# Kernel tuning notes

Hardware: AMD Instinct MI355X
Metric: run time of the kernel (lower is better)

Reference implementation:

```python
import jax, jax.numpy as jnp
import numpy as np

FEAT_STRIDE = 16
PRE_NMS_TOP_N = 6000
POST_NMS_TOP_N = 300
NMS_THRESH = 0.7
MIN_SIZE = 16.0
SCALES = np.array([8.0, 16.0, 32.0])
RATIOS = np.array([0.5, 1.0, 2.0])


def _whctrs(a):
    w = a[2] - a[0] + 1.0
    h = a[3] - a[1] + 1.0
    return w, h, a[0] + 0.5 * (w - 1.0), a[1] + 0.5 * (h - 1.0)


def _mkanchors(ws, hs, xc, yc):
    ws = np.asarray(ws).reshape(-1, 1)
    hs = np.asarray(hs).reshape(-1, 1)
    return np.hstack([xc - 0.5 * (ws - 1.0), yc - 0.5 * (hs - 1.0),
                      xc + 0.5 * (ws - 1.0), yc + 0.5 * (hs - 1.0)])


def generate_anchors(base_size, ratios, scales):
    base = np.array([1.0, 1.0, base_size, base_size]) - 1.0
    w, h, xc, yc = _whctrs(base)
    size = w * h
    ws = np.round(np.sqrt(size / ratios))
    hs = np.round(ws * ratios)
    ratio_anchors = _mkanchors(ws, hs, xc, yc)
    out = []
    for i in range(ratio_anchors.shape[0]):
        w, h, xc, yc = _whctrs(ratio_anchors[i])
        out.append(_mkanchors(w * scales, h * scales, xc, yc))
    return np.vstack(out)


def _nms(boxes, scores, thresh, max_out):
    # greedy NMS, boxes [N,4], scores [N] (-inf = invalid). Returns idx [max_out], valid [max_out]
    N = boxes.shape[0]
    x1, y1, x2, y2 = boxes[:, 0], boxes[:, 1], boxes[:, 2], boxes[:, 3]
    areas = (x2 - x1 + 1.0) * (y2 - y1 + 1.0)
    ar = jnp.arange(N)

    def step(s, _):
        i = jnp.argmax(s)
        valid = s[i] > -jnp.inf
        b = boxes[i]
        xx1 = jnp.maximum(b[0], x1)
        yy1 = jnp.maximum(b[1], y1)
        xx2 = jnp.minimum(b[2], x2)
        yy2 = jnp.minimum(b[3], y2)
        inter = jnp.maximum(0.0, xx2 - xx1 + 1.0) * jnp.maximum(0.0, yy2 - yy1 + 1.0)
        iou = inter / (areas[i] + areas - inter)
        sup = (iou > thresh) | (ar == i)
        return jnp.where(sup, -jnp.inf, s), (i, valid)

    _, (idx, valid) = jax.lax.scan(step, scores, None, length=max_out)
    return idx, valid


def setup_inputs() -> dict:
    key = jax.random.key(0)
    k1, k2 = jax.random.split(key)
    B, A, Hf, Wf = 16, 9, 160, 160
    scores_map = jax.random.uniform(k1, (B, 2 * A, Hf, Wf), dtype=jnp.float32)
    bbox_deltas = jax.random.normal(k2, (B, 4 * A, Hf, Wf), dtype=jnp.float32) * 0.2
    im_info = jnp.tile(jnp.array([[Hf * FEAT_STRIDE, Wf * FEAT_STRIDE, 1.0]], jnp.float32), (B, 1))
    return {"scores_map": scores_map, "bbox_deltas": bbox_deltas, "im_info": im_info}


def reference(scores_map, bbox_deltas, im_info):
    anchors0 = jnp.asarray(generate_anchors(16, RATIOS, SCALES), jnp.float32)  # [A,4]
    A = anchors0.shape[0]
    B, _, Hf, Wf = scores_map.shape
    # fg scores: [B, A, H, W] -> [B, H*W*A]
    scores = scores_map[:, A:].transpose(0, 2, 3, 1).reshape(B, -1)
    deltas = bbox_deltas.transpose(0, 2, 3, 1).reshape(B, -1, 4)  # [B, H*W*A, 4]
    sx = (jnp.arange(Wf) * FEAT_STRIDE).astype(jnp.float32)
    sy = (jnp.arange(Hf) * FEAT_STRIDE).astype(jnp.float32)
    SX, SY = jnp.meshgrid(sx, sy)  # [H, W]
    shifts = jnp.stack([SX.ravel(), SY.ravel(), SX.ravel(), SY.ravel()], axis=1)  # [K,4]
    all_anchors = (shifts[:, None, :] + anchors0[None, :, :]).reshape(-1, 4)  # [K*A, 4]

    aw = all_anchors[:, 2] - all_anchors[:, 0] + 1.0
    ah = all_anchors[:, 3] - all_anchors[:, 1] + 1.0
    acx = all_anchors[:, 0] + 0.5 * aw
    acy = all_anchors[:, 1] + 0.5 * ah

    def single(s, d, info):
        # bbox_transform_inv
        pcx = d[:, 0] * aw + acx
        pcy = d[:, 1] * ah + acy
        pw = jnp.exp(d[:, 2]) * aw
        ph = jnp.exp(d[:, 3]) * ah
        x1 = jnp.clip(pcx - 0.5 * pw, 0.0, info[1] - 1.0)
        y1 = jnp.clip(pcy - 0.5 * ph, 0.0, info[0] - 1.0)
        x2 = jnp.clip(pcx + 0.5 * pw, 0.0, info[1] - 1.0)
        y2 = jnp.clip(pcy + 0.5 * ph, 0.0, info[0] - 1.0)
        boxes = jnp.stack([x1, y1, x2, y2], axis=1)
        ms = MIN_SIZE * info[2]
        keep = ((x2 - x1 + 1.0) >= ms) & ((y2 - y1 + 1.0) >= ms)
        s = jnp.where(keep, s, -jnp.inf)
        top_s, top_i = jax.lax.top_k(s, PRE_NMS_TOP_N)
        top_b = boxes[top_i]
        idx, valid = _nms(top_b, top_s, NMS_THRESH, POST_NMS_TOP_N)
        return jnp.where(valid[:, None], top_b[idx], 0.0)  # [POST, 4]

    out_boxes = jax.vmap(single)(scores, deltas, im_info)  # [B, POST, 4]
    batch_col = jnp.broadcast_to(
        jnp.arange(B, dtype=out_boxes.dtype)[:, None, None], (B, POST_NMS_TOP_N, 1))
    return jnp.concatenate([batch_col, out_boxes], axis=2)  # [B, POST, 5]
```

## Files before the change

kernel.cpp:

```cpp
#include <hip/hip_runtime.h>
#include <cstdint>
#include <cstddef>

typedef unsigned int u32;
typedef unsigned short u16;
typedef unsigned long long u64;

#define NBATCH 16
#define NA 9
#define HF 160
#define WF 160
#define HWC (HF*WF)
#define NPB (NA*HWC)
#define PRE_N 6000
#define POST_N 300
#define SEL_CAP 8192
#define NBIN 2048
#define UNI_BINS 2048
#define NMS_W 16
#define CHUNK 512

__constant__ float c_AW[9] = {184.f,368.f,736.f,128.f,256.f,512.f,88.f,176.f,352.f};
__constant__ float c_AH[9] = {96.f,192.f,384.f,128.f,256.f,512.f,176.f,352.f,704.f};

__device__ __forceinline__ void box_core(
    float d0, float d1, float d2, float d3, int a, int x, int y,
    float imH, float imW, float ms,
    float& x1, float& y1, float& x2, float& y2, bool& keep)
{
  float aw = c_AW[a], ah = c_AH[a];
  float acx = (float)x * 16.0f + 8.0f;
  float acy = (float)y * 16.0f + 8.0f;
  float pcx = d0 * aw + acx;
  float pcy = d1 * ah + acy;
  float pw  = expf(d2) * aw;
  float ph  = expf(d3) * ah;
  x1 = fminf(fmaxf(pcx - 0.5f * pw, 0.0f), imW - 1.0f);
  y1 = fminf(fmaxf(pcy - 0.5f * ph, 0.0f), imH - 1.0f);
  x2 = fminf(fmaxf(pcx + 0.5f * pw, 0.0f), imW - 1.0f);
  y2 = fminf(fmaxf(pcy + 0.5f * ph, 0.0f), imH - 1.0f);
  keep = ((x2 - x1 + 1.0f) >= ms) && ((y2 - y1 + 1.0f) >= ms);
}

__device__ __forceinline__ void box_from_deltas(
    const float* __restrict__ bd, int b, int a, int pos,
    float imH, float imW, float ms,
    float& x1, float& y1, float& x2, float& y2, bool& keep)
{
  int y = pos / WF;
  int x = pos - y * WF;
  size_t base = ((size_t)(b * 4 * NA) + 4 * a) * HWC + (size_t)pos;
  float d0 = bd[base];
  float d1 = bd[base + HWC];
  float d2 = bd[base + 2 * HWC];
  float d3 = bd[base + 3 * HWC];
  box_core(d0, d1, d2, d3, a, x, y, imH, imW, ms, x1, y1, x2, y2, keep);
}

__device__ __forceinline__ u32 desc_enc(float s) {
  u32 su = __float_as_uint(s);
  u32 asc = (su & 0x80000000u) ? ~su : (su | 0x80000000u);
  return ~asc;
}

__device__ __forceinline__ bool iou_gt(float inter, float uni) {
  float ss = fmaf(0.7f, uni, -inter);
  if (fabsf(ss) <= uni * 1e-6f) return (inter / uni > 0.7f);
  return ss < 0.0f;
}

__global__ void __launch_bounds__(256) k_scores_hist(
    const float* __restrict__ sm, const float* __restrict__ bd,
    const float* __restrict__ info, u32* __restrict__ keys, u32* __restrict__ hist) {
  __shared__ u32 lh[UNI_BINS];
  int img   = blockIdx.x / 45;
  int rem   = blockIdx.x - img * 45;
  int a     = rem / 5;
  int chunk = rem - a * 5;
  int tid = threadIdx.x;
  for (int i = tid; i < UNI_BINS; i += 256) lh[i] = 0;
  __syncthreads();
  float imH = info[img*3+0], imW = info[img*3+1], ms = 16.0f * info[img*3+2];
  const float* sp = sm + ((size_t)(img * 2 * NA) + NA + a) * HWC;
  const float* dp = bd + ((size_t)(img * 4 * NA) + 4 * a) * HWC;
  u32* kp = keys + (size_t)img * NPB + (size_t)a * HWC;
  for (int j = 0; j < 5; j++) {
    int pos0 = (chunk * 1280 + j * 256 + tid) * 4;
    float4 s4  = *(const float4*)&sp[pos0];
    float4 q0  = *(const float4*)&dp[pos0];
    float4 q1  = *(const float4*)&dp[HWC + pos0];
    float4 q2  = *(const float4*)&dp[2*HWC + pos0];
    float4 q3  = *(const float4*)&dp[3*HWC + pos0];
    float sv[4] = {s4.x, s4.y, s4.z, s4.w};
    float v0[4] = {q0.x, q0.y, q0.z, q0.w};
    float v1[4] = {q1.x, q1.y, q1.z, q1.w};
    float v2[4] = {q2.x, q2.y, q2.z, q2.w};
    float v3[4] = {q3.x, q3.y, q3.z, q3.w};
    u32 kq[4];
    #pragma unroll
    for (int e = 0; e < 4; e++) {
      int pos = pos0 + e;
      int y = pos / WF;
      int x = pos - y * WF;
      float x1, y1, x2, y2; bool keep;
      box_core(v0[e], v1[e], v2[e], v3[e], a, x, y, imH, imW, ms, x1, y1, x2, y2, keep);
      float s = sv[e];
      if (!keep) s = __uint_as_float(0xFF800000u);
      kq[e] = desc_enc(s);
      int q = (int)floorf(s * (float)UNI_BINS);
      q = q < 0 ? 0 : (q > UNI_BINS - 1 ? UNI_BINS - 1 : q);
      atomicAdd(&lh[(UNI_BINS - 1) - q], 1u);
    }
    *(uint4*)&kp[pos0] = make_uint4(kq[0], kq[1], kq[2], kq[3]);
  }
  __syncthreads();
  u32* gh = hist + img * UNI_BINS;
  for (int i = tid; i < UNI_BINS; i += 256) { u32 v = lh[i]; if (v) atomicAdd(&gh[i], v); }
}

__global__ void __launch_bounds__(256) k_select(
    const u32* __restrict__ keys, const u32* __restrict__ hist, u64* __restrict__ thresh_arr) {
  int img = blockIdx.x, tid = threadIdx.x;
  __shared__ u32 sc[256];
  __shared__ u32 lh[NBIN];
  __shared__ u64 sh_thresh;
  __shared__ int sh_state;
  __shared__ u64 sh_prefix;
  __shared__ u32 sh_kth;
  const u32* gh = hist + img * UNI_BINS;
  u32 loc[8]; u32 tot = 0;
  for (int j = 0; j < 8; j++) { loc[j] = gh[tid * 8 + j]; tot += loc[j]; }
  if (tid == 0) { sh_state = 0; sh_prefix = 0; sh_kth = PRE_N; }
  sc[tid] = tot;
  __syncthreads();
  for (int off = 1; off < 256; off <<= 1) {
    u32 v = sc[tid]; u32 a = (tid >= off) ? sc[tid - off] : 0u;
    __syncthreads(); sc[tid] = v + a; __syncthreads();
  }
  u32 incl = sc[tid], excl = incl - tot;
  if (PRE_N > excl && PRE_N <= incl) {
    u32 run = excl;
    for (int j = 0; j < 8; j++) {
      run += loc[j];
      if (run >= PRE_N) {
        int b = tid * 8 + j;
        if (b < UNI_BINS - 1 && run <= SEL_CAP) {
          float sb = (float)(UNI_BINS - 1 - b) * (1.0f / (float)UNI_BINS);
          sh_thresh = ((u64)desc_enc(sb) << 32) | 0xFFFFFFFFull;
          sh_state = 1;
        }
        break;
      }
    }
  }
  __syncthreads();
  if (!sh_state) {
    const u32* kp = keys + (size_t)img * NPB;
    const int shifts[6] = {53, 42, 31, 20, 9, 0};
    const int widths[6] = {11, 11, 11, 11, 11, 9};
    for (int p = 0; p < 6; p++) {
      if (sh_state) break;
      for (int i = tid; i < NBIN; i += 256) lh[i] = 0;
      __syncthreads();
      u64 prefix = sh_prefix; u32 kth = sh_kth;
      int shift = shifts[p], width = widths[p];
      u32 nb = 1u << width;
      int hs = shift + width;
      for (int i = tid; i < NPB; i += 256) {
        int a = i / HWC;
        int pos = i - a * HWC;
        u64 key = ((u64)kp[i] << 32) | (u64)(u32)(pos * NA + a);
        bool m = (p == 0) || ((key >> hs) == prefix);
        if (m) atomicAdd(&lh[(u32)(key >> shift) & (nb - 1u)], 1u);
      }
      __syncthreads();
      u32 l2[8]; u32 t2 = 0;
      for (int j = 0; j < 8; j++) {
        u32 b = (u32)(tid * 8 + j);
        u32 v = (b < nb) ? lh[b] : 0u;
        l2[j] = v; t2 += v;
      }
      sc[tid] = t2; __syncthreads();
      for (int off = 1; off < 256; off <<= 1) {
        u32 v = sc[tid]; u32 a = (tid >= off) ? sc[tid - off] : 0u;
        __syncthreads(); sc[tid] = v + a; __syncthreads();
      }
      u32 incl2 = sc[tid], excl2 = incl2 - t2;
      if (kth > excl2 && kth <= incl2) {
        u32 run = excl2;
        for (int j = 0; j < 8; j++) {
          run += l2[j];
          if (run >= kth) {
            u32 bin = (u32)(tid * 8 + j);
            u32 below = run - l2[j];
            u32 cnt = l2[j];
            u32 knew = kth - below;
            u64 pfull = (prefix << width) | (u64)bin;
            u32 M = (u32)PRE_N - knew + cnt;
            if (M <= SEL_CAP) {
              u64 lowmask = (shift > 0) ? ((1ULL << shift) - 1ULL) : 0ULL;
              sh_thresh = (pfull << shift) | lowmask;
              sh_state = 1;
            } else {
              sh_prefix = pfull; sh_kth = knew;
            }
            break;
          }
        }
      }
      __syncthreads();
    }
  }
  if (tid == 0) thresh_arr[img] = sh_thresh;
}

__global__ void __launch_bounds__(256) k_compact(
    const u32* __restrict__ keys, const u64* __restrict__ thresh,
    u32* __restrict__ selcnt, u64* __restrict__ sel,
    const float* __restrict__ bd, const float* __restrict__ info,
    float4* __restrict__ boxsel) {
  int img = blockIdx.y;
  int tid = threadIdx.x;
  u64 T = thresh[img];
  int t0 = blockIdx.x * 3840;
  const u32* kp = keys + (size_t)img * NPB + t0;
  u64 fk[15];
  u32 mycnt = 0;
  #pragma unroll
  for (int j = 0; j < 15; j++) {
    int t = t0 + j * 256 + tid;
    u32 d = kp[j * 256 + tid];
    int a = t / HWC;
    int pos = t - a * HWC;
    u64 key = ((u64)d << 32) | (u64)(u32)(pos * NA + a);
    fk[j] = key;
    if (key <= T) mycnt++;
  }
  __shared__ u32 sc[256];
  __shared__ u32 sbase;
  sc[tid] = mycnt;
  __syncthreads();
  for (int off = 1; off < 256; off <<= 1) {
    u32 v = sc[tid];
    u32 add = (tid >= off) ? sc[tid - off] : 0u;
    __syncthreads();
    sc[tid] = v + add;
    __syncthreads();
  }
  if (tid == 255 && sc[255] > 0) sbase = atomicAdd(&selcnt[img], sc[255]);
  __syncthreads();
  if (mycnt == 0) return;
  u32 myoff = sbase + sc[tid] - mycnt;
  u64* sp = sel + (size_t)img * SEL_CAP;
  float4* bp = boxsel + (size_t)img * SEL_CAP;
  float imH = info[img*3+0], imW = info[img*3+1], ms = 16.0f * info[img*3+2];
  u32 c = 0;
  #pragma unroll
  for (int j = 0; j < 15; j++) {
    u64 key = fk[j];
    if (key <= T) {
      u32 p = myoff + c;
      if (p < SEL_CAP) {
        u32 desc = (u32)(key >> 32);
        u32 idx = (u32)key;
        sp[p] = ((u64)desc << 31) | ((u64)idx << 13) | (u64)p;
        int a = (int)(idx % NA);
        int pos = (int)(idx / NA);
        float x1, y1, x2, y2; bool keep;
        box_from_deltas(bd, img, a, pos, imH, imW, ms, x1, y1, x2, y2, keep);
        bp[p] = make_float4(x1, y1, x2, y2);
      }
      c++;
    }
  }
}

__global__ void __launch_bounds__(256) k_sort1(u64* __restrict__ sel, const u32* __restrict__ selcnt) {
  __shared__ u64 s[CHUNK];
  int img = blockIdx.y, c = blockIdx.x, tid = threadIdx.x;
  u32 cnt = selcnt[img]; if (cnt > SEL_CAP) cnt = SEL_CAP;
  u64* sp = sel + (size_t)img * SEL_CAP + (size_t)c * CHUNK;
  int gbase = c * CHUNK;
  for (int i = tid; i < CHUNK; i += 256) s[i] = ((u32)(gbase + i) < cnt) ? sp[i] : ~0ULL;
  __syncthreads();
  for (int k = 2; k <= CHUNK; k <<= 1) {
    for (int j = k >> 1; j > 0; j >>= 1) {
      for (int i = tid; i < CHUNK; i += 256) {
        int p = i ^ j;
        if (p > i) {
          u64 a = s[i], b = s[p];
          bool up = ((i & k) == 0);
          if (up ? (a > b) : (a < b)) { s[i] = b; s[p] = a; }
        }
      }
      __syncthreads();
    }
  }
  for (int i = tid; i < CHUNK; i += 256) sp[i] = s[i];
}

__global__ void __launch_bounds__(1024) k_sort2nms(
    const u64* __restrict__ sel, const u32* __restrict__ selcnt,
    const float4* __restrict__ boxsel, float* __restrict__ out) {
  union SB {
    u64 s[SEL_CAP];
    struct {
      u16 slot16[PRE_N + 64];
      float4 kbox[POST_N];
      float karea[POST_N];
      u64 kcodeW[(POST_N + 7) / 8];
      float4 cb[2][64];
      float car[2][64];
      int cint[2][64];
      u64 wcol[2][64];
      u64 supw[2][NMS_W];
    } n;
  };
  __shared__ SB u;
  __shared__ int sh_nv;
  __shared__ int sh_nkept;
  int img = blockIdx.x;
  int tid = threadIdx.x;
  const u64* sp = sel + (size_t)img * SEL_CAP;
  if (tid == 0) { sh_nv = PRE_N; sh_nkept = 0; }
  for (int i = tid; i < SEL_CAP; i += 1024) u.s[i] = sp[i];
  __syncthreads();
  int d0 = tid * 8;
  for (int L = CHUNK; L < SEL_CAP; L <<= 1) {
    int pairBase = d0 & ~(2 * L - 1);
    int d = d0 - pairBase;
    const u64* A = u.s + pairBase;
    const u64* B = u.s + pairBase + L;
    int lo = d - L; if (lo < 0) lo = 0;
    int hi = (d < L) ? d : L;
    while (lo < hi) {
      int mid = (lo + hi) >> 1;
      if (A[mid] <= B[d - 1 - mid]) lo = mid + 1; else hi = mid;
    }
    int ia = lo, ib = d - lo;
    u64 o[8];
    #pragma unroll
    for (int k = 0; k < 8; k++) {
      bool ta = (ib >= L) || (ia < L && A[ia] <= B[ib]);
      o[k] = ta ? A[ia++] : B[ib++];
    }
    __syncthreads();
    #pragma unroll
    for (int k = 0; k < 8; k++) u.s[d0 + k] = o[k];
    __syncthreads();
  }
  u64 rv[6];
  {
    int k = 0;
    for (int r = tid; r < PRE_N; r += 1024, k++) rv[k] = u.s[r];
    __syncthreads();
    k = 0;
    for (int r = tid; r < PRE_N; r += 1024, k++) {
      u64 key = rv[k];
      u32 desc = (u32)(key >> 31);
      bool valid = desc < 0xFF800000u;
      if (!valid) atomicMin(&sh_nv, r);
      u.n.slot16[r] = valid ? (u16)(key & 0x1FFFu) : (u16)0xFFFF;
    }
  }
  __syncthreads();
  int lane = tid & 63;
  int wv = tid >> 6;
  int nvalid = sh_nv;
  if (nvalid > PRE_N) nvalid = PRE_N;
  const float4* bp = boxsel + (size_t)img * SEL_CAP;
  if (tid < 64) {
    float4 c = make_float4(0.f, 0.f, 0.f, 0.f);
    if (tid < nvalid) { u16 sl = u.n.slot16[tid]; c = bp[sl]; }
    u.n.cb[0][tid] = c;
    float A = (c.z - c.x + 1.0f) * (c.w - c.y + 1.0f);
    u.n.car[0][tid] = A;
    u.n.cint[0][tid] = (int)rintf(8.0f * log2f(A));
  } else if (tid < 128) {
    u.n.wcol[0][tid - 64] = 0;
  } else if (tid < 128 + NMS_W) {
    u.n.supw[0][tid - 128] = 0;
  }
  __syncthreads();
  int pb = 0;
  for (int base = 0; base < nvalid; base += 64, pb ^= 1) {
    int nk = sh_nkept;
    if (nk >= POST_N) break;
    int bn = nvalid - base; if (bn > 64) bn = 64;
    bool sup;
    u64 colpart = 0;
    {
      bool inb = lane < bn;
      sup = !inb;
      if (inb) {
        float4 C = u.n.cb[pb][lane];
        float A0 = u.n.car[pb][lane];
        int myc = u.n.cint[pb][lane];
        int nw = (nk + 7) >> 3;
        for (int jw = wv; jw < nw; jw += NMS_W) {
          u64 w = u.n.kcodeW[jw];
          int jbase = jw << 3;
          int jm = nk - jbase; if (jm > 8) jm = 8;
          for (int k = 0; k < jm; k++) {
            int d = (int)((w >> (k * 8)) & 0xFFu) - myc;
            if (d > 5 || d < -5) continue;
            int j = jbase + k;
            float4 K = u.n.kbox[j];
            float xx1 = fmaxf(K.x, C.x);
            float yy1 = fmaxf(K.y, C.y);
            float xx2 = fminf(K.z, C.z);
            float yy2 = fminf(K.w, C.w);
            float iw = fmaxf(0.0f, xx2 - xx1 + 1.0f);
            float ih = fmaxf(0.0f, yy2 - yy1 + 1.0f);
            float inter = iw * ih;
            float uni = (u.n.karea[j] + A0) - inter;
            sup = sup | iou_gt(inter, uni);
          }
        }
        for (int i = wv; i < lane; i += NMS_W) {
          if (i >= bn) break;
          float Ai = u.n.car[pb][i];
          if (Ai <= 0.6999f * A0 || A0 <= 0.6999f * Ai) continue;
          float4 I4 = u.n.cb[pb][i];
          float xx1 = fmaxf(I4.x, C.x);
          float yy1 = fmaxf(I4.y, C.y);
          float xx2 = fminf(I4.z, C.z);
          float yy2 = fminf(I4.w, C.w);
          float iw = fmaxf(0.0f, xx2 - xx1 + 1.0f);
          float ih = fmaxf(0.0f, yy2 - yy1 + 1.0f);
          float inter = iw * ih;
          float uni = (Ai + A0) - inter;
          if (iou_gt(inter, uni)) colpart |= 1ULL << i;
        }
      }
    }
    u64 bm = __ballot(sup);
    if (lane == 0) u.n.supw[pb][wv] = bm;
    if (colpart) atomicOr(&u.n.wcol[pb][lane], colpart);
    __syncthreads();
    if (wv == 0) {
      u64 so = (lane < NMS_W) ? u.n.supw[pb][lane] : 0ULL;
      so |= __shfl_xor(so, 1);
      so |= __shfl_xor(so, 2);
      so |= __shfl_xor(so, 4);
      so |= __shfl_xor(so, 8);
      so = __shfl(so, 0);
      u64 validm = (bn >= 64) ? ~0ULL : ((1ULL << bn) - 1ULL);
      u64 colm = u.n.wcol[pb][lane];
      u64 live = validm & ~so;
      u64 km = 0;
      int cnt = nk;
      while (live && cnt < POST_N) {
        int c = __ffsll((long long)live) - 1;
        km |= 1ULL << c;
        cnt++;
        u64 dead = __ballot((colm >> c) & 1ULL);
        live &= ~dead;
        live &= ~(1ULL << c);
      }
      if ((km >> lane) & 1ULL) {
        int rank = nk + (int)__popcll(km & ((1ULL << lane) - 1ULL));
        float4 C = u.n.cb[pb][lane];
        u.n.kbox[rank] = C;
        u.n.karea[rank] = u.n.car[pb][lane];
        ((unsigned char*)u.n.kcodeW)[rank] = (unsigned char)u.n.cint[pb][lane];
        float* o = out + ((size_t)img * POST_N + rank) * 5;
        o[0] = (float)img; o[1] = C.x; o[2] = C.y; o[3] = C.z; o[4] = C.w;
      }
      if (lane == 0) sh_nkept = cnt;
    } else if (wv == 1) {
      int nb2 = base + 64;
      if (nb2 < nvalid) {
        int i = nb2 + lane;
        float4 c = make_float4(0.f, 0.f, 0.f, 0.f);
        if (i < nvalid) { u16 sl = u.n.slot16[i]; c = bp[sl]; }
        u.n.cb[pb ^ 1][lane] = c;
        float A = (c.z - c.x + 1.0f) * (c.w - c.y + 1.0f);
        u.n.car[pb ^ 1][lane] = A;
        u.n.cint[pb ^ 1][lane] = (int)rintf(8.0f * log2f(A));
      }
    } else if (wv == 2) {
      u.n.wcol[pb ^ 1][lane] = 0;
      if (lane < NMS_W) u.n.supw[pb ^ 1][lane] = 0;
    }
    __syncthreads();
  }
  int fk = sh_nkept;
  for (int r = fk + tid; r < POST_N; r += NMS_W * 64) {
    float* o = out + ((size_t)img * POST_N + r) * 5;
    o[0] = (float)img; o[1] = 0.f; o[2] = 0.f; o[3] = 0.f; o[4] = 0.f;
  }
}

extern "C" void kernel_launch(void* const* d_in, const int* in_sizes, int n_in,
                              void* d_out, int out_size, void* d_ws, size_t ws_size,
                              hipStream_t stream) {
  const float* sm   = (const float*)d_in[0];
  const float* bd   = (const float*)d_in[1];
  const float* info = (const float*)d_in[2];
  float* out = (float*)d_out;
  char* ws = (char*)d_ws;

  size_t off = 0;
  auto alloc = [&](size_t bytes) { size_t o = off; off += (bytes + 255) & ~(size_t)255; return o; };
  u32* keys     = (u32*)(ws + alloc((size_t)NBATCH * NPB * 4));
  size_t off_hist = alloc((size_t)NBATCH * UNI_BINS * 4);
  u32* hist     = (u32*)(ws + off_hist);
  u32* selcnt   = (u32*)(ws + alloc(NBATCH * 4));
  size_t zero_end = off;
  u64* thresh   = (u64*)(ws + alloc(NBATCH * 8));
  u64* sel      = (u64*)(ws + alloc((size_t)NBATCH * SEL_CAP * 8));
  float4* boxsel= (float4*)(ws + alloc((size_t)NBATCH * SEL_CAP * 16));
  (void)ws_size; (void)in_sizes; (void)n_in; (void)out_size;

  hipMemsetAsync(ws + off_hist, 0, zero_end - off_hist, stream);
  hipLaunchKernelGGL(k_scores_hist, dim3(720), dim3(256), 0, stream, sm, bd, info, keys, hist);
  hipLaunchKernelGGL(k_select, dim3(16), dim3(256), 0, stream, keys, hist, thresh);
  hipLaunchKernelGGL(k_compact, dim3(60, 16), dim3(256), 0, stream, keys, thresh, selcnt, sel, bd, info, boxsel);
  hipLaunchKernelGGL(k_sort1, dim3(SEL_CAP / CHUNK, 16), dim3(256), 0, stream, sel, selcnt);
  hipLaunchKernelGGL(k_sort2nms, dim3(16), dim3(1024), 0, stream, sel, selcnt, boxsel, out);
}
```

Before: 211.7 us.

## Fuse threshold select into histogram kernel, parallelize NMS keep resolution, trim merge work

The separate k_select kernel is folded into k_scores_hist. The last block to finish for each image, detected with an atomic ticket counter, computes the top-k threshold, which saves one kernel launch and its dependency gap. The final merge pass skips threads whose output lies beyond PRE_N. The NMS prefetch of the next candidate tile now starts before the IoU work and is stored afterwards, overlapping global loads with compute. The serial per-candidate keep loop is replaced by a fixed-point ballot iteration with popcount-based truncation. The fused select adds a tail where one block per image runs serially after the histogram, and the fixed-point keep rule must reproduce greedy order exactly.

```diff
diff --git a/kernel.cpp b/kernel.cpp
--- a/kernel.cpp
+++ b/kernel.cpp
@@ -19,6 +19,7 @@
 #define UNI_BINS 2048
 #define NMS_W 16
 #define CHUNK 512
+#define HBLK 45
 
 __constant__ float c_AW[9] = {184.f,368.f,736.f,128.f,256.f,512.f,88.f,176.f,352.f};
 __constant__ float c_AH[9] = {96.f,192.f,384.f,128.f,256.f,512.f,176.f,352.f,704.f};
@@ -71,10 +72,17 @@
 
 __global__ void __launch_bounds__(256) k_scores_hist(
     const float* __restrict__ sm, const float* __restrict__ bd,
-    const float* __restrict__ info, u32* __restrict__ keys, u32* __restrict__ hist) {
+    const float* __restrict__ info, u32* __restrict__ keys, u32* __restrict__ hist,
+    u32* __restrict__ done, u64* __restrict__ thresh_arr) {
   __shared__ u32 lh[UNI_BINS];
-  int img   = blockIdx.x / 45;
-  int rem   = blockIdx.x - img * 45;
+  __shared__ u32 sc[256];
+  __shared__ int sh_ticket;
+  __shared__ u64 sh_thresh;
+  __shared__ int sh_state;
+  __shared__ u64 sh_prefix;
+  __shared__ u32 sh_kth;
+  int img   = blockIdx.x / HBLK;
+  int rem   = blockIdx.x - img * HBLK;
   int a     = rem / 5;
   int chunk = rem - a * 5;
   int tid = threadIdx.x;
@@ -116,26 +124,19 @@
   __syncthreads();
   u32* gh = hist + img * UNI_BINS;
   for (int i = tid; i < UNI_BINS; i += 256) { u32 v = lh[i]; if (v) atomicAdd(&gh[i], v); }
-}
-
-__global__ void __launch_bounds__(256) k_select(
-    const u32* __restrict__ keys, const u32* __restrict__ hist, u64* __restrict__ thresh_arr) {
-  int img = blockIdx.x, tid = threadIdx.x;
-  __shared__ u32 sc[256];
-  __shared__ u32 lh[NBIN];
-  __shared__ u64 sh_thresh;
-  __shared__ int sh_state;
-  __shared__ u64 sh_prefix;
-  __shared__ u32 sh_kth;
-  const u32* gh = hist + img * UNI_BINS;
+  __threadfence();
+  if (tid == 0) sh_ticket = (int)atomicAdd(&done[img], 1u);
+  __syncthreads();
+  if (sh_ticket != HBLK - 1) return;
+  __threadfence();
   u32 loc[8]; u32 tot = 0;
-  for (int j = 0; j < 8; j++) { loc[j] = gh[tid * 8 + j]; tot += loc[j]; }
+  for (int j = 0; j < 8; j++) { loc[j] = atomicAdd(&gh[tid * 8 + j], 0u); tot += loc[j]; }
   if (tid == 0) { sh_state = 0; sh_prefix = 0; sh_kth = PRE_N; }
   sc[tid] = tot;
   __syncthreads();
   for (int off = 1; off < 256; off <<= 1) {
-    u32 v = sc[tid]; u32 a = (tid >= off) ? sc[tid - off] : 0u;
-    __syncthreads(); sc[tid] = v + a; __syncthreads();
+    u32 v = sc[tid]; u32 aa = (tid >= off) ? sc[tid - off] : 0u;
+    __syncthreads(); sc[tid] = v + aa; __syncthreads();
   }
   u32 incl = sc[tid], excl = incl - tot;
   if (PRE_N > excl && PRE_N <= incl) {
@@ -155,7 +156,7 @@
   }
   __syncthreads();
   if (!sh_state) {
-    const u32* kp = keys + (size_t)img * NPB;
+    const u32* kk = keys + (size_t)img * NPB;
     const int shifts[6] = {53, 42, 31, 20, 9, 0};
     const int widths[6] = {11, 11, 11, 11, 11, 9};
     for (int p = 0; p < 6; p++) {
@@ -167,9 +168,9 @@
       u32 nb = 1u << width;
       int hs = shift + width;
       for (int i = tid; i < NPB; i += 256) {
-        int a = i / HWC;
-        int pos = i - a * HWC;
-        u64 key = ((u64)kp[i] << 32) | (u64)(u32)(pos * NA + a);
+        int ia = i / HWC;
+        int pos = i - ia * HWC;
+        u64 key = ((u64)kk[i] << 32) | (u64)(u32)(pos * NA + ia);
         bool m = (p == 0) || ((key >> hs) == prefix);
         if (m) atomicAdd(&lh[(u32)(key >> shift) & (nb - 1u)], 1u);
       }
@@ -182,8 +183,8 @@
       }
       sc[tid] = t2; __syncthreads();
       for (int off = 1; off < 256; off <<= 1) {
-        u32 v = sc[tid]; u32 a = (tid >= off) ? sc[tid - off] : 0u;
-        __syncthreads(); sc[tid] = v + a; __syncthreads();
+        u32 v = sc[tid]; u32 aa = (tid >= off) ? sc[tid - off] : 0u;
+        __syncthreads(); sc[tid] = v + aa; __syncthreads();
       }
       u32 incl2 = sc[tid], excl2 = incl2 - t2;
       if (kth > excl2 && kth <= incl2) {
@@ -327,26 +328,31 @@
   __syncthreads();
   int d0 = tid * 8;
   for (int L = CHUNK; L < SEL_CAP; L <<= 1) {
-    int pairBase = d0 & ~(2 * L - 1);
-    int d = d0 - pairBase;
-    const u64* A = u.s + pairBase;
-    const u64* B = u.s + pairBase + L;
-    int lo = d - L; if (lo < 0) lo = 0;
-    int hi = (d < L) ? d : L;
-    while (lo < hi) {
-      int mid = (lo + hi) >> 1;
-      if (A[mid] <= B[d - 1 - mid]) lo = mid + 1; else hi = mid;
-    }
-    int ia = lo, ib = d - lo;
+    bool act = (2 * L < SEL_CAP) || (d0 < PRE_N);
     u64 o[8];
-    #pragma unroll
-    for (int k = 0; k < 8; k++) {
-      bool ta = (ib >= L) || (ia < L && A[ia] <= B[ib]);
-      o[k] = ta ? A[ia++] : B[ib++];
-    }
-    __syncthreads();
-    #pragma unroll
-    for (int k = 0; k < 8; k++) u.s[d0 + k] = o[k];
+    if (act) {
+      int pairBase = d0 & ~(2 * L - 1);
+      int d = d0 - pairBase;
+      const u64* A = u.s + pairBase;
+      const u64* B = u.s + pairBase + L;
+      int lo = d - L; if (lo < 0) lo = 0;
+      int hi = (d < L) ? d : L;
+      while (lo < hi) {
+        int mid = (lo + hi) >> 1;
+        if (A[mid] <= B[d - 1 - mid]) lo = mid + 1; else hi = mid;
+      }
+      int ia = lo, ib = d - lo;
+      #pragma unroll
+      for (int k = 0; k < 8; k++) {
+        bool ta = (ib >= L) || (ia < L && A[ia] <= B[ib]);
+        o[k] = ta ? A[ia++] : B[ib++];
+      }
+    }
+    __syncthreads();
+    if (act) {
+      #pragma unroll
+      for (int k = 0; k < 8; k++) u.s[d0 + k] = o[k];
+    }
     __syncthreads();
   }
   u64 rv[6];
@@ -387,6 +393,12 @@
     int nk = sh_nkept;
     if (nk >= POST_N) break;
     int bn = nvalid - base; if (bn > 64) bn = 64;
+    float4 pfc = make_float4(0.f, 0.f, 0.f, 0.f);
+    bool havepf = (wv == 1) && (base + 64 < nvalid);
+    if (havepf) {
+      int i = base + 64 + lane;
+      if (i < nvalid) { u16 sl = u.n.slot16[i]; pfc = bp[sl]; }
+    }
     bool sup;
     u64 colpart = 0;
     {
@@ -437,6 +449,12 @@
     u64 bm = __ballot(sup);
     if (lane == 0) u.n.supw[pb][wv] = bm;
     if (colpart) atomicOr(&u.n.wcol[pb][lane], colpart);
+    if (havepf) {
+      u.n.cb[pb ^ 1][lane] = pfc;
+      float A = (pfc.z - pfc.x + 1.0f) * (pfc.w - pfc.y + 1.0f);
+      u.n.car[pb ^ 1][lane] = A;
+      u.n.cint[pb ^ 1][lane] = (int)rintf(8.0f * log2f(A));
+    }
     __syncthreads();
     if (wv == 0) {
       u64 so = (lane < NMS_W) ? u.n.supw[pb][lane] : 0ULL;
@@ -448,18 +466,22 @@
       u64 validm = (bn >= 64) ? ~0ULL : ((1ULL << bn) - 1ULL);
       u64 colm = u.n.wcol[pb][lane];
       u64 live = validm & ~so;
-      u64 km = 0;
-      int cnt = nk;
-      while (live && cnt < POST_N) {
-        int c = __ffsll((long long)live) - 1;
-        km |= 1ULL << c;
-        cnt++;
-        u64 dead = __ballot((colm >> c) & 1ULL);
-        live &= ~dead;
-        live &= ~(1ULL << c);
-      }
-      if ((km >> lane) & 1ULL) {
-        int rank = nk + (int)__popcll(km & ((1ULL << lane) - 1ULL));
+      u64 K = live;
+      while (true) {
+        u64 supk = __ballot((K & colm) != 0ULL);
+        u64 Kn = live & ~supk;
+        if (Kn == K) break;
+        K = Kn;
+      }
+      int m = POST_N - nk;
+      int kc = (int)__popcll(K);
+      if (kc > m) {
+        for (int e = kc - m; e > 0; --e) K &= ~(1ULL << (63 - __clzll((long long)K)));
+        kc = m;
+      }
+      int cnt = nk + kc;
+      if ((K >> lane) & 1ULL) {
+        int rank = nk + (int)__popcll(K & ((1ULL << lane) - 1ULL));
         float4 C = u.n.cb[pb][lane];
         u.n.kbox[rank] = C;
         u.n.karea[rank] = u.n.car[pb][lane];
@@ -468,17 +490,6 @@
         o[0] = (float)img; o[1] = C.x; o[2] = C.y; o[3] = C.z; o[4] = C.w;
       }
       if (lane == 0) sh_nkept = cnt;
-    } else if (wv == 1) {
-      int nb2 = base + 64;
-      if (nb2 < nvalid) {
-        int i = nb2 + lane;
-        float4 c = make_float4(0.f, 0.f, 0.f, 0.f);
-        if (i < nvalid) { u16 sl = u.n.slot16[i]; c = bp[sl]; }
-        u.n.cb[pb ^ 1][lane] = c;
-        float A = (c.z - c.x + 1.0f) * (c.w - c.y + 1.0f);
-        u.n.car[pb ^ 1][lane] = A;
-        u.n.cint[pb ^ 1][lane] = (int)rintf(8.0f * log2f(A));
-      }
     } else if (wv == 2) {
       u.n.wcol[pb ^ 1][lane] = 0;
       if (lane < NMS_W) u.n.supw[pb ^ 1][lane] = 0;
@@ -507,6 +518,7 @@
   size_t off_hist = alloc((size_t)NBATCH * UNI_BINS * 4);
   u32* hist     = (u32*)(ws + off_hist);
   u32* selcnt   = (u32*)(ws + alloc(NBATCH * 4));
+  u32* done     = (u32*)(ws + alloc(NBATCH * 4));
   size_t zero_end = off;
   u64* thresh   = (u64*)(ws + alloc(NBATCH * 8));
   u64* sel      = (u64*)(ws + alloc((size_t)NBATCH * SEL_CAP * 8));
@@ -514,8 +526,8 @@
   (void)ws_size; (void)in_sizes; (void)n_in; (void)out_size;
 
   hipMemsetAsync(ws + off_hist, 0, zero_end - off_hist, stream);
-  hipLaunchKernelGGL(k_scores_hist, dim3(720), dim3(256), 0, stream, sm, bd, info, keys, hist);
-  hipLaunchKernelGGL(k_select, dim3(16), dim3(256), 0, stream, keys, hist, thresh);
+  hipLaunchKernelGGL(k_scores_hist, dim3(NBATCH * HBLK), dim3(256), 0, stream,
+                     sm, bd, info, keys, hist, done, thresh);
   hipLaunchKernelGGL(k_compact, dim3(60, 16), dim3(256), 0, stream, keys, thresh, selcnt, sel, bd, info, boxsel);
   hipLaunchKernelGGL(k_sort1, dim3(SEL_CAP / CHUNK, 16), dim3(256), 0, stream, sel, selcnt);
   hipLaunchKernelGGL(k_sort2nms, dim3(16), dim3(1024), 0, stream, sel, selcnt, boxsel, out);
```

New measurement: 276.0 us. +30.3%, slower.
